# Performance work log

Hardware: AMD Instinct MI355X
Metric: run time of the kernel (lower is better)

Reference implementation:

```python
import jax, jax.numpy as jnp
import numpy as np

P = 5  # patchsize == stride (non-overlapping)


def unfold_patches(x, p):
    # x: [N, C, H, W] -> [N, L, C, p, p], blocks ordered row-major (matches F.unfold)
    N, C, H, W = x.shape
    x = x.reshape(N, C, H // p, p, W // p, p)
    return x.transpose(0, 2, 4, 1, 3, 5).reshape(N, (H // p) * (W // p), C, p, p)


def fold_patches(pat, H, W, p):
    # [N, L, C, p, p] -> [N, C, H, W]; stride==kernel so F.fold is pure placement (no overlap sums)
    N, L, C, _, _ = pat.shape
    x = pat.reshape(N, H // p, W // p, C, p, p)
    return x.transpose(0, 3, 1, 4, 2, 5).reshape(N, C, H, W)


def gather_scale_concat(fold, idx, gamma):
    # fold: [N, L, C, p, p]; idx: [N, L, 4] int; gamma: [4]
    def gath(k):
        return jnp.take_along_axis(fold, idx[:, :, k][:, :, None, None, None], axis=1)
    # first slot uses patch j itself (not idx[...,0]), per the original loop body
    return jnp.concatenate(
        [gamma[0] * fold, gamma[1] * gath(1), gamma[2] * gath(2), gamma[3] * gath(3)], axis=2)


def conv3x3(x, w, b):
    y = jax.lax.conv_general_dilated(x, w, window_strides=(1, 1), padding='SAME',
                                     dimension_numbers=('NCHW', 'OIHW', 'NCHW'))
    return y + b[None, :, None, None]


def setup_inputs() -> dict:
    key = jax.random.key(0)
    ks = jax.random.split(key, 7)
    N, C, H, W = 4, 32, 300, 300
    L = (H // P) * (W // P)
    x_rgb = jax.random.normal(ks[0], (N, C, H, W), dtype=jnp.float32)
    y_hsi = jax.random.normal(ks[1], (N, C, H, W), dtype=jnp.float32)
    corr = jax.random.randint(ks[2], (2, N, L, 4), 0, L)
    rgb_gamma = jnp.ones((4,), jnp.float32)
    hsi_gamma = jnp.ones((4,), jnp.float32)
    rgb_W = jax.random.normal(ks[3], (C, 4 * C, 3, 3), dtype=jnp.float32) * 0.02
    rgb_b = jnp.zeros((C,), jnp.float32)
    hsi_W = jax.random.normal(ks[4], (C, 4 * C, 3, 3), dtype=jnp.float32) * 0.02
    hsi_b = jnp.zeros((C,), jnp.float32)
    return {'x_rgb': x_rgb, 'y_hsi': y_hsi, 'corr': corr,
            'rgb_gamma': rgb_gamma, 'hsi_gamma': hsi_gamma,
            'rgb_W': rgb_W, 'rgb_b': rgb_b, 'hsi_W': hsi_W, 'hsi_b': hsi_b}


def reference(x_rgb, y_hsi, corr, rgb_gamma, hsi_gamma, rgb_W, rgb_b, hsi_W, hsi_b):
    n_feats = x_rgb.shape[1]
    half = n_feats // 2
    H, W = x_rgb.shape[2], x_rgb.shape[3]
    hsi = jnp.concatenate([x_rgb[:, :half], y_hsi[:, :half]], axis=1)      # [N, n_feats, H, W]
    rgb = jnp.concatenate([x_rgb[:, half:n_feats], y_hsi[:, half:n_feats]], axis=1)
    idx = corr[0]  # [N, L, 4]
    # H, W divisible by P -> calc_padding yields zero padding
    fold_rgb = unfold_patches(rgb, P)  # [N, L, C, p, p]
    fold_hsi = unfold_patches(hsi, P)
    patch_rgb = gather_scale_concat(fold_rgb, idx, rgb_gamma)  # [N, L, 4C, p, p]
    patch_hsi = gather_scale_concat(fold_hsi, idx, hsi_gamma)
    img_rgb = fold_patches(patch_rgb, H, W, P)  # [N, 4C, H, W]
    img_hsi = fold_patches(patch_hsi, H, W, P)
    out_rgb = conv3x3(img_rgb, rgb_W, rgb_b) + rgb
    out_hsi = conv3x3(img_hsi, hsi_W, hsi_b) + hsi
    return (out_rgb, out_hsi)
```

## Files before the change

### kernel.cpp

```cpp
#include <hip/hip_runtime.h>

#define HW        90000
#define OUT_HALF  11520000
#define CPLANE    11520000ull
#define WPACK_OFF  46080000ull
#define ZOFF       46227456
#define JB_OFF     46227520
#define WS_NEED    (46227520ull + 230400ull)

typedef short short4v __attribute__((ext_vector_type(4)));
typedef short short8 __attribute__((ext_vector_type(8)));
typedef int   int4v  __attribute__((ext_vector_type(4)));
typedef float f32x4  __attribute__((ext_vector_type(4)));
typedef unsigned int u32;

__device__ inline short f2bf(float f) {
    unsigned u = __builtin_bit_cast(unsigned, f);
    u += 0x7fff + ((u >> 16) & 1);
    return (short)(u >> 16);
}
__device__ inline float bf2f(short s) {
    unsigned u = ((unsigned)(unsigned short)s) << 16;
    return __builtin_bit_cast(float, u);
}
__device__ inline void gload16(char* ldst, const char* gsrc) {
    __builtin_amdgcn_global_load_lds(
        (const __attribute__((address_space(1))) u32*)gsrc,
        (__attribute__((address_space(3))) u32*)ldst, 16, 0, 0);
}

__global__ __launch_bounds__(256)
void pack_weights(const float* __restrict__ wR, const float* __restrict__ wH,
                  const float* __restrict__ rg, const float* __restrict__ hg,
                  short* __restrict__ wpack) {
    int id = blockIdx.x * 256 + threadIdx.x;
    if (id >= 73728) return;
    int e    = id & 7;
    int lane = (id >> 3) & 63;
    int h    = (id >> 9) & 1;
    int t    = (id >> 10) % 9;
    int kb   = ((id >> 10) / 9) & 3;
    int conv = id / 36864;
    int co   = h * 16 + (lane & 15);
    int cin  = kb * 32 + (lane >> 4) * 8 + e;
    const float* w = conv ? wH : wR;
    const float* g = conv ? hg : rg;
    wpack[id] = f2bf(w[(co * 128 + cin) * 9 + t] * g[cin >> 5]);
}

__global__ __launch_bounds__(256)
void pack_jb(const int* __restrict__ corr, int* __restrict__ jb) {
    int id = blockIdx.x * 256 + threadIdx.x;
    if (id >= 57600) return;
    int k = id & 3, j = (id >> 2) % 3600, n = id / 14400;
    int jp = (k == 0) ? j : corr[(n * 3600 + j) * 4 + k];
    jb[id] = ((jp / 60) * 1500 + (jp % 60) * 5) * 64;
}

__global__ __launch_bounds__(256)
void nchw2nhwc(const float* __restrict__ xrgb, const float* __restrict__ yhsi,
               short* __restrict__ cmb) {
    int wave = threadIdx.x >> 6, lane = threadIdx.x & 63;
    if (lane >= 60) return;
    int y = blockIdx.y * 4 + wave;
    int x = blockIdx.x * 60 + lane;
    int n = blockIdx.z;
    const float* xb = xrgb + n * 32 * HW + y * 300 + x;
    const float* yb = yhsi + n * 32 * HW + y * 300 + x;
    size_t pxo = ((size_t)n * HW + y * 300 + x) * 32;
    short* d0 = cmb + pxo;
    short* d1 = cmb + CPLANE + pxo;
    #pragma unroll
    for (int q = 0; q < 4; ++q) {
        short8 v0, v1;
        #pragma unroll
        for (int e = 0; e < 8; ++e) {
            int c = q * 8 + e;
            v0[e] = f2bf((c < 16) ? xb[(16 + c) * HW] : yb[c * HW]);
            v1[e] = f2bf((c < 16) ? xb[c * HW] : yb[(c - 16) * HW]);
        }
        *(short8*)(d0 + q * 8) = v0;
        *(short8*)(d1 + q * 8) = v1;
    }
}

__global__ __launch_bounds__(256, 3)
void conv_mfma(const char* __restrict__ wsbase, const short* __restrict__ wpack,
               const float* __restrict__ bR, const float* __restrict__ bH,
               float* __restrict__ out) {
    __shared__ alignas(16) char lds[2][21504];
    int tile = blockIdx.x;
    int n = blockIdx.y;
    int conv = blockIdx.z;
    int ty = tile / 19, tx = tile - ty * 19;
    int y0 = ty * 16, x0 = tx * 16;
    int tid = threadIdx.x;
    int wave = tid >> 6, lane = tid & 63;

    const short* cmb = (const short*)wsbase + conv * CPLANE + (size_t)n * HW * 32;
    const short* wp  = wpack + conv * 36864;
    int cmb_byte = (int)(conv * (CPLANE * 2)) + n * (HW * 64);
    const int* jbtab = (const int*)(wsbase + JB_OFF);

    int soffB[6][4];
    #pragma unroll
    for (int ji = 0; ji < 6; ++ji) {
        int j4 = wave + ji * 4;
        #pragma unroll
        for (int k = 0; k < 4; ++k) soffB[ji][k] = ZOFF;
        if (j4 < 21) {
            int off = j4 * 1024 + lane * 16;
            int pxp = off >> 6;
            int pxl = pxp ^ ((pxp >> 2) & 1);
            int cl  = ((off >> 4) & 3) ^ (pxl & 3);
            int cb  = cl * 16;
            #pragma unroll
            for (int k = 0; k < 4; ++k) soffB[ji][k] = ZOFF + cb;
            if (pxl < 324) {
                int hr = pxl / 18, hc = pxl - hr * 18;
                int gy = y0 + hr - 1, gx = x0 + hc - 1;
                if (gy >= 0 && gy < 300 && gx >= 0 && gx < 300) {
                    int pr = gy / 5, pc = gx / 5;
                    int j  = pr * 60 + pc;
                    int intra = (gy - pr * 5) * 300 + (gx - pc * 5);
                    int4v jbv = *(const int4v*)(jbtab + (n * 3600 + j) * 4);
                    int base = cmb_byte + intra * 64 + cb;
                    soffB[ji][0] = base + jbv[0];
                    soffB[ji][1] = base + jbv[1];
                    soffB[ji][2] = base + jbv[2];
                    soffB[ji][3] = base + jbv[3];
                }
            }
        }
    }

    #define STAGE(buf, k)                                                        \
        do {                                                                     \
            _Pragma("unroll")                                                    \
            for (int ji = 0; ji < 6; ++ji) {                                     \
                int j4 = wave + ji * 4;                                          \
                if (j4 < 21)                                                     \
                    gload16(&lds[buf][j4 * 1024], wsbase + soffB[ji][(k)]);      \
            }                                                                    \
        } while (0)

    int l15 = lane & 15, lh = lane >> 4;
    int wr = wave * 4;

    int boff[3][6];
    #pragma unroll
    for (int dxi = 0; dxi < 3; ++dxi)
        #pragma unroll
        for (int rr = 0; rr < 6; ++rr) {
            int hp = (wr + rr) * 18 + (l15 + dxi);
            boff[dxi][rr] = (hp * 64 + lh * 16) ^ ((hp & 7) << 4);
        }

    STAGE(0, 0);
    __syncthreads();

    f32x4 acc[4][2];
    #pragma unroll
    for (int g = 0; g < 4; ++g)
        #pragma unroll
        for (int h = 0; h < 2; ++h)
            acc[g][h] = (f32x4){0.f, 0.f, 0.f, 0.f};

    #pragma unroll
    for (int kb = 0; kb < 4; ++kb) {
        short8 a[3][3][2];
        #pragma unroll
        for (int dxi = 0; dxi < 3; ++dxi)
            #pragma unroll
            for (int dyi = 0; dyi < 3; ++dyi) {
                int t = dyi * 3 + dxi;
                a[dxi][dyi][0] = *(const short8*)(wp + (((kb * 9 + t) * 2 + 0) * 64 + lane) * 8);
                a[dxi][dyi][1] = *(const short8*)(wp + (((kb * 9 + t) * 2 + 1) * 64 + lane) * 8);
            }
        __builtin_amdgcn_sched_barrier(0);
        if (kb == 0) STAGE(1, 1);
        if (kb == 1) STAGE(0, 2);
        if (kb == 2) STAGE(1, 3);
        __builtin_amdgcn_sched_barrier(0);
        const char* base = lds[kb & 1];
        __builtin_amdgcn_s_setprio(1);
        #pragma unroll
        for (int dxi = 0; dxi < 3; ++dxi) {
            short8 b[6];
            #pragma unroll
            for (int rr = 0; rr < 6; ++rr)
                b[rr] = *(const short8*)(base + boff[dxi][rr]);
            #pragma unroll
            for (int g = 0; g < 4; ++g) {
                #pragma unroll
                for (int dyi = 0; dyi < 3; ++dyi) {
                    acc[g][0] = __builtin_amdgcn_mfma_f32_16x16x32_bf16(a[dxi][dyi][0], b[g + dyi], acc[g][0], 0, 0, 0);
                    acc[g][1] = __builtin_amdgcn_mfma_f32_16x16x32_bf16(a[dxi][dyi][1], b[g + dyi], acc[g][1], 0, 0, 0);
                }
            }
        }
        __builtin_amdgcn_s_setprio(0);
        if (kb < 3) __syncthreads();
    }

    const float* bias = conv ? bH : bR;
    float bia[2][4];
    #pragma unroll
    for (int h = 0; h < 2; ++h)
        #pragma unroll
        for (int reg = 0; reg < 4; ++reg)
            bia[h][reg] = bias[h * 16 + lh * 4 + reg];
    #pragma unroll
    for (int g = 0; g < 4; ++g) {
        int gy = y0 + wr + g;
        int gx = x0 + l15;
        if (gy < 300 && gx < 300) {
            int pixo = gy * 300 + gx;
            const short* resp = cmb + (size_t)pixo * 32 + lh * 4;
            #pragma unroll
            for (int h = 0; h < 2; ++h) {
                short4v r = *(const short4v*)(resp + h * 16);
                #pragma unroll
                for (int reg = 0; reg < 4; ++reg) {
                    int co = h * 16 + lh * 4 + reg;
                    out[conv * OUT_HALF + (n * 32 + co) * HW + pixo]
                        = acc[g][h][reg] + bia[h][reg] + bf2f(r[reg]);
                }
            }
        }
    }
    #undef STAGE
}

__global__ __launch_bounds__(256)
void fused_gather_conv(const float* __restrict__ xrgb, const float* __restrict__ yhsi,
                       const int* __restrict__ corr, const float* __restrict__ rgb_gamma,
                       const float* __restrict__ hsi_gamma, const float* __restrict__ wR,
                       const float* __restrict__ bR, const float* __restrict__ wH,
                       const float* __restrict__ bH, float* __restrict__ out) {
    int tid = blockIdx.x * blockDim.x + threadIdx.x;
    if (tid >= 4 * HW) return;
    int n = tid / HW, pix = tid - n * HW;
    int y = pix / 300, x = pix - y * 300;
    const int* idx = corr + n * (3600 * 4);
    const float* xb = xrgb + n * (32 * HW);
    const float* yb = yhsi + n * (32 * HW);
    float accR[32], accH[32];
    #pragma unroll
    for (int i = 0; i < 32; ++i) { accR[i] = 0.f; accH[i] = 0.f; }
    for (int k = 0; k < 4; ++k) {
        float gr = rgb_gamma[k], gh = hsi_gamma[k];
        int off[9];
        #pragma unroll
        for (int t = 0; t < 9; ++t) {
            int dy = t / 3 - 1, dx = t % 3 - 1;
            int yy = y + dy, xx = x + dx;
            int o = -1;
            if (yy >= 0 && yy < 300 && xx >= 0 && xx < 300) {
                int pr = yy / 5, pc = xx / 5;
                int j = pr * 60 + pc;
                int jp = (k == 0) ? j : idx[j * 4 + k];
                o = ((jp / 60) * 5 + (yy - pr * 5)) * 300 + (jp % 60) * 5 + (xx - pc * 5);
            }
            off[t] = o;
        }
        for (int c = 0; c < 32; ++c) {
            const float* srcR = (c < 16) ? (xb + (16 + c) * HW) : (yb + c * HW);
            const float* srcH = (c < 16) ? (xb + c * HW) : (yb + (c - 16) * HW);
            float vr[9], vh[9];
            #pragma unroll
            for (int t = 0; t < 9; ++t) {
                bool vld = off[t] >= 0;
                vr[t] = vld ? gr * srcR[off[t]] : 0.f;
                vh[t] = vld ? gh * srcH[off[t]] : 0.f;
            }
            const float* wRp = wR + (k * 32 + c) * 9;
            const float* wHp = wH + (k * 32 + c) * 9;
            #pragma unroll
            for (int t = 0; t < 9; ++t)
                #pragma unroll
                for (int co = 0; co < 32; ++co) {
                    accR[co] = fmaf(vr[t], wRp[co * 1152 + t], accR[co]);
                    accH[co] = fmaf(vh[t], wHp[co * 1152 + t], accH[co]);
                }
        }
    }
    #pragma unroll
    for (int co = 0; co < 32; ++co) {
        float resR = (co < 16) ? xb[(16 + co) * HW + pix] : yb[co * HW + pix];
        float resH = (co < 16) ? xb[co * HW + pix] : yb[(co - 16) * HW + pix];
        out[(n * 32 + co) * HW + pix]            = accR[co] + bR[co] + resR;
        out[OUT_HALF + (n * 32 + co) * HW + pix] = accH[co] + bH[co] + resH;
    }
}

extern "C" void kernel_launch(void* const* d_in, const int* in_sizes, int n_in,
                              void* d_out, int out_size, void* d_ws, size_t ws_size,
                              hipStream_t stream) {
    const float* xrgb = (const float*)d_in[0];
    const float* yhsi = (const float*)d_in[1];
    const int*   corr = (const int*)d_in[2];
    const float* rg   = (const float*)d_in[3];
    const float* hg   = (const float*)d_in[4];
    const float* wR   = (const float*)d_in[5];
    const float* bR   = (const float*)d_in[6];
    const float* wH   = (const float*)d_in[7];
    const float* bH   = (const float*)d_in[8];
    float* out = (float*)d_out;

    if (ws_size >= WS_NEED) {
        char* ws = (char*)d_ws;
        hipMemsetAsync(ws + ZOFF, 0, 64, stream);
        hipLaunchKernelGGL(pack_weights, dim3(288), dim3(256), 0, stream,
                           wR, wH, rg, hg, (short*)(ws + WPACK_OFF));
        hipLaunchKernelGGL(pack_jb, dim3(225), dim3(256), 0, stream,
                           corr, (int*)(ws + JB_OFF));
        hipLaunchKernelGGL(nchw2nhwc, dim3(5, 75, 4), dim3(256), 0, stream,
                           xrgb, yhsi, (short*)ws);
        hipLaunchKernelGGL(conv_mfma, dim3(361, 4, 2), dim3(256), 0, stream,
                           (const char*)ws, (const short*)(ws + WPACK_OFF), bR, bH, out);
    } else {
        int total = 4 * HW;
        hipLaunchKernelGGL(fused_gather_conv, dim3((total + 255) / 256), dim3(256), 0, stream,
                           xrgb, yhsi, corr, rg, hg, wR, bR, wH, bH, out);
    }
}
```

Measured before the change: 127.2 us.

## Read identity-slot conv input directly from global memory, skipping LDS staging

The first channel block (the patch's own data, not gathered) was staged through LDS like the three gathered blocks. It now goes through only three LDS stages for the gathered slots. The identity slot is computed at the end with per-lane direct global loads at precomputed offsets, which are contiguous rather than gathered. This removes one LDS stage and one barrier, at the cost of uncached-through-LDS global reads that are redundant across waves (a 3x3 halo is reread per dx), with higher latency that is not overlapped.

```diff
diff --git a/kernel.cpp b/kernel.cpp
--- a/kernel.cpp
+++ b/kernel.cpp
@@ -102,12 +102,15 @@
     int cmb_byte = (int)(conv * (CPLANE * 2)) + n * (HW * 64);
     const int* jbtab = (const int*)(wsbase + JB_OFF);
 
-    int soffB[6][4];
+    int l15 = lane & 15, lh = lane >> 4;
+    int wr = wave * 4;
+
+    int soffB[6][3];
     #pragma unroll
     for (int ji = 0; ji < 6; ++ji) {
         int j4 = wave + ji * 4;
         #pragma unroll
-        for (int k = 0; k < 4; ++k) soffB[ji][k] = ZOFF;
+        for (int k = 0; k < 3; ++k) soffB[ji][k] = ZOFF;
         if (j4 < 21) {
             int off = j4 * 1024 + lane * 16;
             int pxp = off >> 6;
@@ -115,7 +118,7 @@
             int cl  = ((off >> 4) & 3) ^ (pxl & 3);
             int cb  = cl * 16;
             #pragma unroll
-            for (int k = 0; k < 4; ++k) soffB[ji][k] = ZOFF + cb;
+            for (int k = 0; k < 3; ++k) soffB[ji][k] = ZOFF + cb;
             if (pxl < 324) {
                 int hr = pxl / 18, hc = pxl - hr * 18;
                 int gy = y0 + hr - 1, gx = x0 + hc - 1;
@@ -125,14 +128,25 @@
                     int intra = (gy - pr * 5) * 300 + (gx - pc * 5);
                     int4v jbv = *(const int4v*)(jbtab + (n * 3600 + j) * 4);
                     int base = cmb_byte + intra * 64 + cb;
-                    soffB[ji][0] = base + jbv[0];
-                    soffB[ji][1] = base + jbv[1];
-                    soffB[ji][2] = base + jbv[2];
-                    soffB[ji][3] = base + jbv[3];
-                }
-            }
-        }
-    }
+                    soffB[ji][0] = base + jbv[1];
+                    soffB[ji][1] = base + jbv[2];
+                    soffB[ji][2] = base + jbv[3];
+                }
+            }
+        }
+    }
+
+    int goff[3][6];
+    #pragma unroll
+    for (int dxi = 0; dxi < 3; ++dxi)
+        #pragma unroll
+        for (int rr = 0; rr < 6; ++rr) {
+            int gy = y0 + wr + rr - 1;
+            int gx = x0 + l15 + dxi - 1;
+            bool v = (gy >= 0 && gy < 300 && gx >= 0 && gx < 300);
+            goff[dxi][rr] = v ? (cmb_byte + (gy * 300 + gx) * 64 + lh * 16)
+                              : (ZOFF + lh * 16);
+        }
 
     #define STAGE(buf, k)                                                        \
         do {                                                                     \
@@ -144,9 +158,6 @@
             }                                                                    \
         } while (0)
 
-    int l15 = lane & 15, lh = lane >> 4;
-    int wr = wave * 4;
-
     int boff[3][6];
     #pragma unroll
     for (int dxi = 0; dxi < 3; ++dxi)
@@ -167,7 +178,8 @@
             acc[g][h] = (f32x4){0.f, 0.f, 0.f, 0.f};
 
     #pragma unroll
-    for (int kb = 0; kb < 4; ++kb) {
+    for (int ph = 0; ph < 3; ++ph) {
+        const int kb = ph + 1;
         short8 a[3][3][2];
         #pragma unroll
         for (int dxi = 0; dxi < 3; ++dxi)
@@ -178,11 +190,10 @@
                 a[dxi][dyi][1] = *(const short8*)(wp + (((kb * 9 + t) * 2 + 1) * 64 + lane) * 8);
             }
         __builtin_amdgcn_sched_barrier(0);
-        if (kb == 0) STAGE(1, 1);
-        if (kb == 1) STAGE(0, 2);
-        if (kb == 2) STAGE(1, 3);
+        if (ph == 0) STAGE(1, 1);
+        if (ph == 1) STAGE(0, 2);
         __builtin_amdgcn_sched_barrier(0);
-        const char* base = lds[kb & 1];
+        const char* base = lds[ph & 1];
         __builtin_amdgcn_s_setprio(1);
         #pragma unroll
         for (int dxi = 0; dxi < 3; ++dxi) {
@@ -200,7 +211,35 @@
             }
         }
         __builtin_amdgcn_s_setprio(0);
-        if (kb < 3) __syncthreads();
+        if (ph < 2) __syncthreads();
+    }
+
+    {
+        const int kb = 0;
+        __builtin_amdgcn_s_setprio(1);
+        #pragma unroll
+        for (int dxi = 0; dxi < 3; ++dxi) {
+            short8 b[6];
+            #pragma unroll
+            for (int rr = 0; rr < 6; ++rr)
+                b[rr] = *(const short8*)(wsbase + goff[dxi][rr]);
+            short8 a[3][2];
+            #pragma unroll
+            for (int dyi = 0; dyi < 3; ++dyi) {
+                int t = dyi * 3 + dxi;
+                a[dyi][0] = *(const short8*)(wp + (((kb * 9 + t) * 2 + 0) * 64 + lane) * 8);
+                a[dyi][1] = *(const short8*)(wp + (((kb * 9 + t) * 2 + 1) * 64 + lane) * 8);
+            }
+            #pragma unroll
+            for (int g = 0; g < 4; ++g) {
+                #pragma unroll
+                for (int dyi = 0; dyi < 3; ++dyi) {
+                    acc[g][0] = __builtin_amdgcn_mfma_f32_16x16x32_bf16(a[dyi][0], b[g + dyi], acc[g][0], 0, 0, 0);
+                    acc[g][1] = __builtin_amdgcn_mfma_f32_16x16x32_bf16(a[dyi][1], b[g + dyi], acc[g][1], 0, 0, 0);
+                }
+            }
+        }
+        __builtin_amdgcn_s_setprio(0);
     }
 
     const float* bias = conv ? bH : bR;
```

New measurement: 133.8 us. +5.2%, slower.
